# Kernel optimization log

Measured on AMD Instinct MI355X. Metric: run time of the kernel, lower is better.

The kernel has to match this reference:

```python
import jax, jax.numpy as jnp
import numpy as np

DN = ('NCHW', 'OIHW', 'NCHW')


def _conv_bn_relu(x, w, s, b):
    # ConvModule in eval mode: conv(no bias) + BN(running stats, folded to affine) + ReLU
    y = jax.lax.conv_general_dilated(x, w, (1, 1), ((1, 1), (1, 1)), dimension_numbers=DN)
    return jnp.maximum(y * s[None, :, None, None] + b[None, :, None, None], 0.0)


def _head(x, w1, s1, b1, w2, s2, b2, wf, bf):
    y = _conv_bn_relu(x, w1, s1, b1)
    y = _conv_bn_relu(y, w2, s2, b2)
    y = jax.lax.conv_general_dilated(y, wf, (1, 1), ((0, 0), (0, 0)), dimension_numbers=DN)
    return y + bf[None, :, None, None]  # [B, 5, H, W]


def _make_anchors(shapes, strides, offset=0.5):
    pts, sts = [], []
    for (h, w), s in zip(shapes, strides):
        sx = jnp.arange(w, dtype=jnp.float32) + offset
        sy = jnp.arange(h, dtype=jnp.float32) + offset
        yy, xx = jnp.meshgrid(sy, sx, indexing='ij')
        pts.append(jnp.stack((xx, yy), -1).reshape(-1, 2))
        sts.append(jnp.full((h * w, 1), float(s), dtype=jnp.float32))
    # transposed as in the torch code: anchors [2, N], strides [1, N]
    return jnp.concatenate(pts).T, jnp.concatenate(sts).T


def setup_inputs():
    key = jax.random.key(0)
    ks = jax.random.split(key, 16)
    B = 8
    cfg = {'p3': (128, 160), 'p4': (256, 80), 'p5': (512, 40)}
    inp = {}
    i = 0
    for name, (C, HW) in cfg.items():
        inp[name] = jax.random.normal(ks[i], (B, C, HW, HW), dtype=jnp.float32)
        i += 1
    for name, (C, HW) in cfg.items():
        fan3 = 1.0 / float(np.sqrt(C * 9))
        fan1 = 1.0 / float(np.sqrt(C))
        inp[f'w1_{name}'] = jax.random.normal(ks[i], (C, C, 3, 3), jnp.float32) * fan3; i += 1
        inp[f's1_{name}'] = jnp.ones((C,), jnp.float32)
        inp[f'b1_{name}'] = jnp.zeros((C,), jnp.float32)
        inp[f'w2_{name}'] = jax.random.normal(ks[i], (C, C, 3, 3), jnp.float32) * fan3; i += 1
        inp[f's2_{name}'] = jnp.ones((C,), jnp.float32)
        inp[f'b2_{name}'] = jnp.zeros((C,), jnp.float32)
        inp[f'wf_{name}'] = jax.random.normal(ks[i], (5, C, 1, 1), jnp.float32) * fan1; i += 1
        inp[f'bf_{name}'] = jnp.zeros((5,), jnp.float32)
    return inp


def reference(p3, p4, p5,
              w1_p3, s1_p3, b1_p3, w2_p3, s2_p3, b2_p3, wf_p3, bf_p3,
              w1_p4, s1_p4, b1_p4, w2_p4, s2_p4, b2_p4, wf_p4, bf_p4,
              w1_p5, s1_p5, b1_p5, w2_p5, s2_p5, b2_p5, wf_p5, bf_p5):
    y3 = _head(p3, w1_p3, s1_p3, b1_p3, w2_p3, s2_p3, b2_p3, wf_p3, bf_p3)
    y4 = _head(p4, w1_p4, s1_p4, b1_p4, w2_p4, s2_p4, b2_p4, wf_p4, bf_p4)
    y5 = _head(p5, w1_p5, s1_p5, b1_p5, w2_p5, s2_p5, b2_p5, wf_p5, bf_p5)
    feats = [y3, y4, y5]
    B = p3.shape[0]
    shapes = [(f.shape[2], f.shape[3]) for f in feats]
    anchors, strides = _make_anchors(shapes, (8, 16, 32))  # [2,N], [1,N]
    out = jnp.concatenate([f.reshape(B, 5, -1) for f in feats], axis=2)  # [B,5,N]
    box, cls = out[:, :4], out[:, 4:5]
    anc = anchors[None]  # [1,2,N]
    lt, rb = box[:, :2], box[:, 2:4]
    x1y1 = anc - lt
    x2y2 = anc + rb
    box = jnp.concatenate(((x1y1 + x2y2) * 0.5, x2y2 - x1y1), axis=1) * strides[None]
    return jnp.concatenate((box, jax.nn.sigmoid(cls)), axis=1)  # [B,5,N] pre-NMS detections
```

## Files before the change

kernel.cpp:

```cpp
#include <hip/hip_runtime.h>
#include <stdint.h>

typedef short short8 __attribute__((ext_vector_type(8)));
typedef float f32x16 __attribute__((ext_vector_type(16)));

template<int I> struct IC { static constexpr int value = I; };

__device__ __forceinline__ uint16_t f2bf(float f){
  union{float f;uint32_t u;}v; v.f=f;
  uint32_t u=v.u; u += 0x7fffu + ((u>>16)&1u);
  return (uint16_t)(u>>16);
}
__device__ __forceinline__ float bf2f(uint16_t h){
  union{uint32_t u;float f;}v; v.u=((uint32_t)h)<<16; return v.f;
}

__device__ __forceinline__ void gl_lds16(const void* g, void* l){
  __builtin_amdgcn_global_load_lds((__attribute__((address_space(1))) const void*)g,
                                   (__attribute__((address_space(3))) void*)l, 16, 0, 0);
}

__global__ __launch_bounds__(256) void prep_w(const float* __restrict__ w,
                                              const float* __restrict__ s,
                                              uint16_t* __restrict__ dst, int C){
  int idx = blockIdx.x*256 + threadIdx.x;
  int total = C*C*9;
  if (idx >= total) return;
  int tap = idx % 9; int t = idx/9;
  int ci = t % C; int co = t / C;
  float val = w[idx]*s[co];
  int KB = C>>5;
  int f = co>>5;
  int lane = (co&31) | (((ci>>3)&1)<<5);
  int kk = (ci>>4)&1, kb = ci>>5, j = ci&7;
  size_t off = ((((size_t)(f*KB + kb)*9 + tap)*2 + kk)*64 + lane)*8 + j;
  dst[off] = f2bf(val);
}

template<int C,int H>
__global__ __launch_bounds__(256) void pad_in(const float* __restrict__ x, uint16_t* __restrict__ xp){
  constexpr int W=H, Hp=H+2, Wp=W+2, KB=C/32;
  int idx = blockIdx.x*256 + threadIdx.x;
  int total = 8*KB*Hp*Wp;
  if (idx >= total) return;
  int w = idx % Wp; int t2 = idx / Wp;
  int h = t2 % Hp;  int bk = t2 / Hp;
  const uint32_t key = (uint32_t)((w&7)<<4);
  char* dst = (char*)xp;
  size_t cbyte = (size_t)idx*64;
  if (h==0 || h==Hp-1 || w==0 || w==Wp-1){
    uint4 z = {0,0,0,0};
#pragma unroll
    for (int q=0;q<4;++q) *(uint4*)(dst + ((cbyte + (uint32_t)(q*16)) ^ key)) = z;
  } else {
    const int b = bk/KB, kb = bk - b*KB;
    const float* src = x + (((size_t)(b*C + kb*32)*H + (h-1))*W + (w-1));
#pragma unroll
    for (int q=0;q<4;++q){
      uint16_t tmp[8];
#pragma unroll
      for (int j=0;j<8;++j) tmp[j] = f2bf(src[(size_t)(q*8+j)*(H*W)]);
      *(uint4*)(dst + ((cbyte + (uint32_t)(q*16)) ^ key)) = *(uint4*)tmp;
    }
  }
}

template<int C,int H>
__global__ __launch_bounds__(256) void zero_border(uint16_t* __restrict__ yp){
  constexpr int Hp=H+2, Wp=H+2, KB=C/32;
  constexpr int NB = 2*Wp + 2*(Hp-2);
  int idx = blockIdx.x*256 + threadIdx.x;
  int total = 8*KB*NB;
  if (idx >= total) return;
  int j = idx % NB; int bk = idx / NB;
  int h, w;
  if (j < 2*Wp){ h = (j<Wp)?0:(Hp-1); w = j%Wp; }
  else { int j2 = j - 2*Wp; h = 1 + (j2 % (Hp-2)); w = (j2 < (Hp-2))?0:(Wp-1); }
  size_t chunk = ((size_t)bk*Hp + h)*Wp + w;
  const uint32_t key = (uint32_t)((w&7)<<4);
  uint4 z = {0,0,0,0};
  char* dst = (char*)yp;
#pragma unroll
  for (int q=0;q<4;++q) *(uint4*)(dst + ((chunk*64 + (uint32_t)(q*16)) ^ key)) = z;
}

template<int C,int H,bool PADOUT>
__device__ __forceinline__ void conv_body(int lbid,
    const uint16_t* __restrict__ in, const uint16_t* __restrict__ wq,
    const float* __restrict__ bias, uint16_t* __restrict__ out, char* lds)
{
  constexpr int W=H, Hp=H+2, Wp=W+2, KB=C/32, TW=40, TH=8;
  constexpr int COB=128;
  constexpr int R=TH+2, BUF=R*3072, NT=R*3, WAVES=4;
  const int tid = threadIdx.x, lane = tid&63, wave = tid>>6;
  const int wm = wave>>1, wn = wave&1;
  const int l31 = lane&31, h5 = lane>>5;

  int t = lbid;
  const int cb = t % (C/COB); t /= (C/COB);
  const int wt = t % (W/TW);  t /= (W/TW);
  const int ht = t % (H/TH);
  const int b  = t / (H/TH);
  const int h0 = ht*TH, w0 = wt*TW;
  const int cbCO = cb*(COB/32);

  int addrB[5][3];
#pragma unroll
  for (int ni=0; ni<5; ++ni){
    int s = wn*160 + ni*32 + l31;
    int th = s/40, tw = s - th*40;
#pragma unroll
    for (int dw=0; dw<3; ++dw){
      int col = tw + dw;
      addrB[ni][dw] = th*3072 + ((col*64 + h5*16) ^ ((col&7)<<4));
    }
  }

  const char* wp[2];
#pragma unroll
  for (int mi=0; mi<2; ++mi){
    int f = cbCO + wm*2 + mi;
    wp[mi] = (const char*)wq + (size_t)f * ((size_t)KB*9*2*1024) + lane*16;
  }

  f32x16 acc[2][5];
#pragma unroll
  for (int mi=0;mi<2;++mi)
#pragma unroll
    for (int ni=0;ni<5;++ni)
#pragma unroll
      for (int e=0;e<16;++e) acc[mi][ni][e] = 0.f;

  auto STAGE = [&](int bi, int kb){
    const char* src = (const char*)(in + ((size_t)(b*KB + kb)*Hp + h0)*((size_t)Wp*32) + (size_t)w0*32);
    for (int tt = wave; tt < NT; tt += WAVES){
      int r = tt/3, k = tt - r*3;
      char* l = lds + bi*BUF + r*3072 + k*1024;
      const char* g = src + (size_t)r*(Wp*64) + k*1024 + lane*16;
      if (k < 2 || lane < 40) gl_lds16(g, l);
    }
  };

  auto COMPUTE = [&](auto BC){
    constexpr int BI = decltype(BC)::value;
    const char* lb = lds + BI*BUF;
    short8 wc[2][2], wnx[2][2];
#pragma unroll
    for (int mi=0;mi<2;++mi){
      wc[mi][0] = *(const short8*)(wp[mi]);
      wc[mi][1] = *(const short8*)(wp[mi] + 1024);
      wp[mi] += 2048;
    }
#pragma unroll
    for (int tap=0; tap<9; ++tap){
      const int dh = tap/3, dw = tap - dh*3;
      if (tap < 8){
#pragma unroll
        for (int mi=0;mi<2;++mi){
          wnx[mi][0] = *(const short8*)(wp[mi]);
          wnx[mi][1] = *(const short8*)(wp[mi] + 1024);
          wp[mi] += 2048;
        }
      }
#pragma unroll
      for (int ni=0; ni<5; ++ni){
        const int a0 = addrB[ni][dw] + dh*3072;
        short8 b0 = *(const short8*)(lb + a0);
        short8 b1 = *(const short8*)(lb + (a0 ^ 32));
        acc[0][ni] = __builtin_amdgcn_mfma_f32_32x32x16_bf16(wc[0][0], b0, acc[0][ni], 0,0,0);
        acc[1][ni] = __builtin_amdgcn_mfma_f32_32x32x16_bf16(wc[1][0], b0, acc[1][ni], 0,0,0);
        acc[0][ni] = __builtin_amdgcn_mfma_f32_32x32x16_bf16(wc[0][1], b1, acc[0][ni], 0,0,0);
        acc[1][ni] = __builtin_amdgcn_mfma_f32_32x32x16_bf16(wc[1][1], b1, acc[1][ni], 0,0,0);
      }
      if (tap < 8){
#pragma unroll
        for (int mi=0;mi<2;++mi){ wc[mi][0]=wnx[mi][0]; wc[mi][1]=wnx[mi][1]; }
      }
    }
  };

  STAGE(0, 0);
  __syncthreads();
#pragma unroll 1
  for (int kb = 0; kb < KB; kb += 2){
    STAGE(1, kb+1);
    COMPUTE(IC<0>{});
    __syncthreads();
    if (kb+2 < KB) STAGE(0, kb+2);
    COMPUTE(IC<1>{});
    __syncthreads();
  }

#pragma unroll
  for (int mi=0; mi<2; ++mi){
    const int kbo = cbCO + wm*2 + mi;
#pragma unroll
    for (int ni=0; ni<5; ++ni){
      const int s = wn*160 + ni*32 + l31;
      const int th = s/40, tw = s - th*40;
      size_t chunk; uint32_t key;
      if (PADOUT){
        const int hh = h0+th+1, ww = w0+tw+1;
        chunk = ((size_t)(b*KB + kbo)*Hp + hh)*Wp + ww;
        key = (uint32_t)((ww&7)<<4);
      } else {
        const int hh = h0+th, ww = w0+tw;
        chunk = ((size_t)(b*KB + kbo)*H + hh)*W + ww;
        key = (uint32_t)((ww&7)<<4);
      }
      char* ob = (char*)out;
#pragma unroll
      for (int q=0; q<4; ++q){
        const int cob = kbo*32 + q*8 + h5*4;
        float v0 = fmaxf(acc[mi][ni][4*q+0] + bias[cob+0], 0.f);
        float v1 = fmaxf(acc[mi][ni][4*q+1] + bias[cob+1], 0.f);
        float v2 = fmaxf(acc[mi][ni][4*q+2] + bias[cob+2], 0.f);
        float v3 = fmaxf(acc[mi][ni][4*q+3] + bias[cob+3], 0.f);
        uint2 dd;
        dd.x = (uint32_t)f2bf(v0) | ((uint32_t)f2bf(v1)<<16);
        dd.y = (uint32_t)f2bf(v2) | ((uint32_t)f2bf(v3)<<16);
        *(uint2*)(ob + ((chunk*64 + (uint32_t)(q*16 + h5*8)) ^ key)) = dd;
      }
    }
  }
}

template<bool PADOUT>
__global__ __launch_bounds__(256, 2) void conv_all(int b45, int b34,
    const uint16_t* in5, const uint16_t* wq5, const float* bi5, uint16_t* o5,
    const uint16_t* in4, const uint16_t* wq4, const float* bi4, uint16_t* o4,
    const uint16_t* in3, const uint16_t* wq3, const float* bi3, uint16_t* o3)
{
  __shared__ __align__(16) char lds[61440];
  const int bid = blockIdx.x;
  if (bid < b45)      conv_body<512, 40, PADOUT>(bid,       in5, wq5, bi5, o5, lds);
  else if (bid < b34) conv_body<256, 80, PADOUT>(bid - b45, in4, wq4, bi4, o4, lds);
  else                conv_body<128,160, PADOUT>(bid - b34, in3, wq3, bi3, o3, lds);
}

template<int C,int H,int OFF,int STRIDE>
__global__ __launch_bounds__(256) void head_final(const uint16_t* __restrict__ y,
    const float* __restrict__ wf, const float* __restrict__ bfp, float* __restrict__ outp)
{
  constexpr int W=H, HW=H*W, KBo=C/32, S=33600;
  int idx = blockIdx.x*256 + threadIdx.x;
  if (idx >= 8*HW) return;
  const int b = idx/HW, sp = idx - b*HW;
  const int w = sp % W;
  const uint32_t key = (uint32_t)((w&7)<<4);
  float a0=bfp[0], a1=bfp[1], a2=bfp[2], a3=bfp[3], a4=bfp[4];
  const char* yb = (const char*)y;
  for (int kb=0; kb<KBo; ++kb){
    size_t cbyte = ((size_t)(b*KBo + kb)*HW + sp)*64;
#pragma unroll
    for (int q=0; q<4; ++q){
      uint4 u = *(const uint4*)(yb + ((cbyte + (uint32_t)(q*16)) ^ key));
      const uint16_t* pv = (const uint16_t*)&u;
#pragma unroll
      for (int j=0; j<8; ++j){
        float v = bf2f(pv[j]);
        int ci = kb*32 + q*8 + j;
        a0 += v*wf[0*C+ci]; a1 += v*wf[1*C+ci]; a2 += v*wf[2*C+ci];
        a3 += v*wf[3*C+ci]; a4 += v*wf[4*C+ci];
      }
    }
  }
  const float ax = (float)(sp % W) + 0.5f;
  const float ay = (float)(sp / W) + 0.5f;
  const float o0 = (ax + 0.5f*(a2-a0)) * (float)STRIDE;
  const float o1 = (ay + 0.5f*(a3-a1)) * (float)STRIDE;
  const float o2 = (a0+a2) * (float)STRIDE;
  const float o3 = (a1+a3) * (float)STRIDE;
  const float o4 = 1.0f/(1.0f + expf(-a4));
  float* ob = outp + (size_t)b*5*S + OFF + sp;
  ob[0*S]=o0; ob[1*S]=o1; ob[2*S]=o2; ob[3*S]=o3; ob[4*S]=o4;
}

extern "C" void kernel_launch(void* const* d_in, const int* in_sizes, int n_in,
                              void* d_out, int out_size, void* d_ws, size_t ws_size,
                              hipStream_t stream){
  (void)in_sizes; (void)n_in; (void)out_size;
  const float* x[3] = {(const float*)d_in[0], (const float*)d_in[1], (const float*)d_in[2]};
  const float *w1[3],*s1[3],*b1[3],*w2[3],*s2[3],*b2[3],*wf[3],*bfp[3];
  for (int h=0; h<3; ++h){
    const int base = 3 + h*8;
    w1[h]=(const float*)d_in[base+0]; s1[h]=(const float*)d_in[base+1];
    b1[h]=(const float*)d_in[base+2]; w2[h]=(const float*)d_in[base+3];
    s2[h]=(const float*)d_in[base+4]; b2[h]=(const float*)d_in[base+5];
    wf[h]=(const float*)d_in[base+6]; bfp[h]=(const float*)d_in[base+7];
  }
  static const int   Cs[3] = {128, 256, 512};
  static const size_t Wb[3] = {294912, 1179648, 4718592};
  static const size_t Ab[3] = {53747712, 27541504, 14450688};
  static const int   NB[3] = {640, 320, 160};
  float* out = (float*)d_out;
  char* ws = (char*)d_ws;

  size_t off = 0; size_t wOff[3][2];
  for (int h=0; h<3; ++h) for (int c=0; c<2; ++c){ wOff[h][c]=off; off += Wb[h]; }
  off = (off + 255) & ~(size_t)255;
  size_t aOff[3], bOff[3];
  for (int h=0; h<3; ++h){ aOff[h]=off; off += Ab[h]; }
  for (int h=0; h<3; ++h){ bOff[h]=off; off += Ab[h]; }
  const size_t fusedNeed = off;

  const size_t seqA = (2*4718592 + 255) & ~(size_t)255;
  const size_t seqB = seqA + 53747712;
  const size_t seqNeed = seqB + 53747712;

  if (ws_size >= fusedNeed){
    for (int h=0; h<3; ++h){
      int tot = 9*Cs[h]*Cs[h];
      prep_w<<<(tot+255)/256, 256, 0, stream>>>(w1[h], s1[h], (uint16_t*)(ws+wOff[h][0]), Cs[h]);
      prep_w<<<(tot+255)/256, 256, 0, stream>>>(w2[h], s2[h], (uint16_t*)(ws+wOff[h][1]), Cs[h]);
    }
    pad_in<128,160><<<3281, 256, 0, stream>>>(x[0], (uint16_t*)(ws+aOff[0]));
    pad_in<256, 80><<<1681, 256, 0, stream>>>(x[1], (uint16_t*)(ws+aOff[1]));
    pad_in<512, 40><<< 882, 256, 0, stream>>>(x[2], (uint16_t*)(ws+aOff[2]));
    zero_border<128,160><<<81, 256, 0, stream>>>((uint16_t*)(ws+bOff[0]));
    zero_border<256, 80><<<81, 256, 0, stream>>>((uint16_t*)(ws+bOff[1]));
    zero_border<512, 40><<<82, 256, 0, stream>>>((uint16_t*)(ws+bOff[2]));
    const int b45 = NB[2], b34 = NB[2]+NB[1], grid = NB[2]+NB[1]+NB[0];
    conv_all<true><<<grid, 256, 0, stream>>>(b45, b34,
      (const uint16_t*)(ws+aOff[2]), (const uint16_t*)(ws+wOff[2][0]), b1[2], (uint16_t*)(ws+bOff[2]),
      (const uint16_t*)(ws+aOff[1]), (const uint16_t*)(ws+wOff[1][0]), b1[1], (uint16_t*)(ws+bOff[1]),
      (const uint16_t*)(ws+aOff[0]), (const uint16_t*)(ws+wOff[0][0]), b1[0], (uint16_t*)(ws+bOff[0]));
    conv_all<false><<<grid, 256, 0, stream>>>(b45, b34,
      (const uint16_t*)(ws+bOff[2]), (const uint16_t*)(ws+wOff[2][1]), b2[2], (uint16_t*)(ws+aOff[2]),
      (const uint16_t*)(ws+bOff[1]), (const uint16_t*)(ws+wOff[1][1]), b2[1], (uint16_t*)(ws+aOff[1]),
      (const uint16_t*)(ws+bOff[0]), (const uint16_t*)(ws+wOff[0][1]), b2[0], (uint16_t*)(ws+aOff[0]));
    head_final<128,160,     0,  8><<<800, 256, 0, stream>>>((const uint16_t*)(ws+aOff[0]), wf[0], bfp[0], out);
    head_final<256, 80, 25600, 16><<<200, 256, 0, stream>>>((const uint16_t*)(ws+aOff[1]), wf[1], bfp[1], out);
    head_final<512, 40, 32000, 32><<< 50, 256, 0, stream>>>((const uint16_t*)(ws+aOff[2]), wf[2], bfp[2], out);
  } else {
    if (ws_size < seqNeed) return;
    uint16_t* W1p = (uint16_t*)(ws + 0);
    uint16_t* W2p = (uint16_t*)(ws + 4718592);
    uint16_t* A   = (uint16_t*)(ws + seqA);
    uint16_t* B   = (uint16_t*)(ws + seqB);
    for (int h=0; h<3; ++h){
      int tot = 9*Cs[h]*Cs[h];
      prep_w<<<(tot+255)/256, 256, 0, stream>>>(w1[h], s1[h], W1p, Cs[h]);
      prep_w<<<(tot+255)/256, 256, 0, stream>>>(w2[h], s2[h], W2p, Cs[h]);
      int grid = NB[h];
      int b45, b34;
      if (h==2){ b45=grid; b34=grid; } else if (h==1){ b45=0; b34=grid; } else { b45=0; b34=0; }
      if (h==0){
        pad_in<128,160><<<3281,256,0,stream>>>(x[0], A);
        zero_border<128,160><<<81,256,0,stream>>>(B);
      } else if (h==1){
        pad_in<256,80><<<1681,256,0,stream>>>(x[1], A);
        zero_border<256,80><<<81,256,0,stream>>>(B);
      } else {
        pad_in<512,40><<<882,256,0,stream>>>(x[2], A);
        zero_border<512,40><<<82,256,0,stream>>>(B);
      }
      conv_all<true><<<grid, 256, 0, stream>>>(b45, b34,
        A, W1p, b1[h], B,  A, W1p, b1[h], B,  A, W1p, b1[h], B);
      conv_all<false><<<grid, 256, 0, stream>>>(b45, b34,
        B, W2p, b2[h], A,  B, W2p, b2[h], A,  B, W2p, b2[h], A);
      if (h==0)      head_final<128,160,     0,  8><<<800,256,0,stream>>>(A, wf[0], bfp[0], out);
      else if (h==1) head_final<256, 80, 25600, 16><<<200,256,0,stream>>>(A, wf[1], bfp[1], out);
      else           head_final<512, 40, 32000, 32><<< 50,256,0,stream>>>(A, wf[2], bfp[2], out);
    }
  }
}
```

Measured before the change: 848.1 us.

## Switch conv to 16x16x32 MFMA with smaller tiles and LDS-staged weight prep

Replaces the 32x32x16 bf16 MFMA tiling with 16x16x32 MFMA. Each wave now holds a 4x5 grid of 4-wide accumulators, and the spatial tile height is halved from 8 to 4 rows, which doubles the block count. The weight layout is changed to a tap-major, 16-output-channel-fragment format. A new prep kernel stages weights through LDS and writes packed bf16 pairs. Lower LDS use and fewer accumulator registers allow launch bounds of 3 blocks per CU for more occupancy, at the cost of more halo reloads per output and different MFMA throughput characteristics.

```diff
diff --git a/kernel.cpp b/kernel.cpp
--- a/kernel.cpp
+++ b/kernel.cpp
@@ -2,7 +2,7 @@
 #include <stdint.h>
 
 typedef short short8 __attribute__((ext_vector_type(8)));
-typedef float f32x16 __attribute__((ext_vector_type(16)));
+typedef float f32x4 __attribute__((ext_vector_type(4)));
 
 template<int I> struct IC { static constexpr int value = I; };
 
@@ -20,21 +20,35 @@
                                    (__attribute__((address_space(3))) void*)l, 16, 0, 0);
 }
 
-__global__ __launch_bounds__(256) void prep_w(const float* __restrict__ w,
-                                              const float* __restrict__ s,
-                                              uint16_t* __restrict__ dst, int C){
-  int idx = blockIdx.x*256 + threadIdx.x;
-  int total = C*C*9;
-  if (idx >= total) return;
-  int tap = idx % 9; int t = idx/9;
-  int ci = t % C; int co = t / C;
-  float val = w[idx]*s[co];
-  int KB = C>>5;
-  int f = co>>5;
-  int lane = (co&31) | (((ci>>3)&1)<<5);
-  int kk = (ci>>4)&1, kb = ci>>5, j = ci&7;
-  size_t off = ((((size_t)(f*KB + kb)*9 + tap)*2 + kk)*64 + lane)*8 + j;
-  dst[off] = f2bf(val);
+__global__ __launch_bounds__(256) void prep_w2(const float* __restrict__ w,
+                                               const float* __restrict__ s,
+                                               uint16_t* __restrict__ dst, int C){
+  __shared__ float lds[16][289];
+  const int F16 = C >> 4;
+  const int tid = threadIdx.x;
+  const int f16 = blockIdx.x % F16;
+  const int kb  = blockIdx.x / F16;
+#pragma unroll
+  for (int i = 0; i < 18; ++i){
+    int idx = tid + i*256;
+    int co  = idx / 288, rem = idx - co*288;
+    lds[co][rem] = w[(size_t)(f16*16 + co)*C*9 + (size_t)kb*288 + rem];
+  }
+  __syncthreads();
+  const int lane = tid >> 2;
+  const int jj   = (tid & 3)*2;
+  const int co_l = lane & 15, oct = lane >> 4;
+  const int ci0  = oct*8 + jj;
+  const float sc = s[f16*16 + co_l];
+  uint32_t* db = (uint32_t*)dst;
+#pragma unroll
+  for (int tap = 0; tap < 9; ++tap){
+    float v0 = lds[co_l][(ci0  )*9 + tap] * sc;
+    float v1 = lds[co_l][(ci0+1)*9 + tap] * sc;
+    uint32_t pk = (uint32_t)f2bf(v0) | ((uint32_t)f2bf(v1) << 16);
+    size_t o = (((size_t)(kb*9 + tap)*F16 + f16)*512 + (size_t)lane*8 + jj) >> 1;
+    db[o] = pk;
+  }
 }
 
 template<int C,int H>
@@ -89,12 +103,13 @@
     const uint16_t* __restrict__ in, const uint16_t* __restrict__ wq,
     const float* __restrict__ bias, uint16_t* __restrict__ out, char* lds)
 {
-  constexpr int W=H, Hp=H+2, Wp=W+2, KB=C/32, TW=40, TH=8;
-  constexpr int COB=128;
-  constexpr int R=TH+2, BUF=R*3072, NT=R*3, WAVES=4;
+  constexpr int W=H, Hp=H+2, Wp=W+2, KB=C/32, TW=40, TH=4;
+  constexpr int COB=128, F16B=C/16;
+  constexpr int R=TH+2, ROWB=42*64, BUF=R*ROWB, NT=R*3, WAVES=4;
+  constexpr int TAPSTRIDE = F16B*1024;
   const int tid = threadIdx.x, lane = tid&63, wave = tid>>6;
   const int wm = wave>>1, wn = wave&1;
-  const int l31 = lane&31, h5 = lane>>5;
+  const int l15 = lane&15, h2 = lane>>4;
 
   int t = lbid;
   const int cb = t % (C/COB); t /= (C/COB);
@@ -102,40 +117,38 @@
   const int ht = t % (H/TH);
   const int b  = t / (H/TH);
   const int h0 = ht*TH, w0 = wt*TW;
-  const int cbCO = cb*(COB/32);
 
   int addrB[5][3];
 #pragma unroll
   for (int ni=0; ni<5; ++ni){
-    int s = wn*160 + ni*32 + l31;
+    int s = wn*80 + ni*16 + l15;
     int th = s/40, tw = s - th*40;
 #pragma unroll
     for (int dw=0; dw<3; ++dw){
       int col = tw + dw;
-      addrB[ni][dw] = th*3072 + ((col*64 + h5*16) ^ ((col&7)<<4));
-    }
-  }
-
-  const char* wp[2];
-#pragma unroll
-  for (int mi=0; mi<2; ++mi){
-    int f = cbCO + wm*2 + mi;
-    wp[mi] = (const char*)wq + (size_t)f * ((size_t)KB*9*2*1024) + lane*16;
-  }
-
-  f32x16 acc[2][5];
-#pragma unroll
-  for (int mi=0;mi<2;++mi)
+      addrB[ni][dw] = th*ROWB + ((col*64 + h2*16) ^ ((col&7)<<4));
+    }
+  }
+
+  const char* wp = (const char*)wq + (size_t)(cb*8 + wm*4)*1024 + (size_t)lane*16;
+
+  f32x4 acc[4][5];
+#pragma unroll
+  for (int mi=0;mi<4;++mi)
 #pragma unroll
     for (int ni=0;ni<5;++ni)
-#pragma unroll
-      for (int e=0;e<16;++e) acc[mi][ni][e] = 0.f;
+      acc[mi][ni] = (f32x4){0.f,0.f,0.f,0.f};
+
+  short8 a_[4];
+#pragma unroll
+  for (int mi=0; mi<4; ++mi) a_[mi] = *(const short8*)(wp + mi*1024);
+  wp += TAPSTRIDE;
 
   auto STAGE = [&](int bi, int kb){
     const char* src = (const char*)(in + ((size_t)(b*KB + kb)*Hp + h0)*((size_t)Wp*32) + (size_t)w0*32);
     for (int tt = wave; tt < NT; tt += WAVES){
       int r = tt/3, k = tt - r*3;
-      char* l = lds + bi*BUF + r*3072 + k*1024;
+      char* l = lds + bi*BUF + r*ROWB + k*1024;
       const char* g = src + (size_t)r*(Wp*64) + k*1024 + lane*16;
       if (k < 2 || lane < 40) gl_lds16(g, l);
     }
@@ -144,38 +157,24 @@
   auto COMPUTE = [&](auto BC){
     constexpr int BI = decltype(BC)::value;
     const char* lb = lds + BI*BUF;
-    short8 wc[2][2], wnx[2][2];
-#pragma unroll
-    for (int mi=0;mi<2;++mi){
-      wc[mi][0] = *(const short8*)(wp[mi]);
-      wc[mi][1] = *(const short8*)(wp[mi] + 1024);
-      wp[mi] += 2048;
-    }
 #pragma unroll
     for (int tap=0; tap<9; ++tap){
       const int dh = tap/3, dw = tap - dh*3;
-      if (tap < 8){
-#pragma unroll
-        for (int mi=0;mi<2;++mi){
-          wnx[mi][0] = *(const short8*)(wp[mi]);
-          wnx[mi][1] = *(const short8*)(wp[mi] + 1024);
-          wp[mi] += 2048;
-        }
-      }
-#pragma unroll
-      for (int ni=0; ni<5; ++ni){
-        const int a0 = addrB[ni][dw] + dh*3072;
-        short8 b0 = *(const short8*)(lb + a0);
-        short8 b1 = *(const short8*)(lb + (a0 ^ 32));
-        acc[0][ni] = __builtin_amdgcn_mfma_f32_32x32x16_bf16(wc[0][0], b0, acc[0][ni], 0,0,0);
-        acc[1][ni] = __builtin_amdgcn_mfma_f32_32x32x16_bf16(wc[1][0], b0, acc[1][ni], 0,0,0);
-        acc[0][ni] = __builtin_amdgcn_mfma_f32_32x32x16_bf16(wc[0][1], b1, acc[0][ni], 0,0,0);
-        acc[1][ni] = __builtin_amdgcn_mfma_f32_32x32x16_bf16(wc[1][1], b1, acc[1][ni], 0,0,0);
-      }
-      if (tap < 8){
-#pragma unroll
-        for (int mi=0;mi<2;++mi){ wc[mi][0]=wnx[mi][0]; wc[mi][1]=wnx[mi][1]; }
-      }
+      short8 an_[4];
+#pragma unroll
+      for (int mi=0;mi<4;++mi) an_[mi] = *(const short8*)(wp + mi*1024);
+      wp += TAPSTRIDE;
+      short8 bf[5];
+#pragma unroll
+      for (int ni=0; ni<5; ++ni)
+        bf[ni] = *(const short8*)(lb + addrB[ni][dw] + dh*ROWB);
+#pragma unroll
+      for (int ni=0; ni<5; ++ni)
+#pragma unroll
+        for (int mi=0; mi<4; ++mi)
+          acc[mi][ni] = __builtin_amdgcn_mfma_f32_16x16x32_bf16(a_[mi], bf[ni], acc[mi][ni], 0,0,0);
+#pragma unroll
+      for (int mi=0;mi<4;++mi) a_[mi] = an_[mi];
     }
   };
 
@@ -192,11 +191,13 @@
   }
 
 #pragma unroll
-  for (int mi=0; mi<2; ++mi){
-    const int kbo = cbCO + wm*2 + mi;
+  for (int mi=0; mi<4; ++mi){
+    const int kbo = cb*4 + wm*2 + (mi>>1);
+    const int cobase = kbo*32 + (mi&1)*16 + h2*4;
+    const f32x4 bv = *(const f32x4*)(bias + cobase);
 #pragma unroll
     for (int ni=0; ni<5; ++ni){
-      const int s = wn*160 + ni*32 + l31;
+      const int s = wn*80 + ni*16 + l15;
       const int th = s/40, tw = s - th*40;
       size_t chunk; uint32_t key;
       if (PADOUT){
@@ -208,30 +209,25 @@
         chunk = ((size_t)(b*KB + kbo)*H + hh)*W + ww;
         key = (uint32_t)((ww&7)<<4);
       }
-      char* ob = (char*)out;
-#pragma unroll
-      for (int q=0; q<4; ++q){
-        const int cob = kbo*32 + q*8 + h5*4;
-        float v0 = fmaxf(acc[mi][ni][4*q+0] + bias[cob+0], 0.f);
-        float v1 = fmaxf(acc[mi][ni][4*q+1] + bias[cob+1], 0.f);
-        float v2 = fmaxf(acc[mi][ni][4*q+2] + bias[cob+2], 0.f);
-        float v3 = fmaxf(acc[mi][ni][4*q+3] + bias[cob+3], 0.f);
-        uint2 dd;
-        dd.x = (uint32_t)f2bf(v0) | ((uint32_t)f2bf(v1)<<16);
-        dd.y = (uint32_t)f2bf(v2) | ((uint32_t)f2bf(v3)<<16);
-        *(uint2*)(ob + ((chunk*64 + (uint32_t)(q*16 + h5*8)) ^ key)) = dd;
-      }
+      float v0 = fmaxf(acc[mi][ni][0] + bv[0], 0.f);
+      float v1 = fmaxf(acc[mi][ni][1] + bv[1], 0.f);
+      float v2 = fmaxf(acc[mi][ni][2] + bv[2], 0.f);
+      float v3 = fmaxf(acc[mi][ni][3] + bv[3], 0.f);
+      uint2 dd;
+      dd.x = (uint32_t)f2bf(v0) | ((uint32_t)f2bf(v1)<<16);
+      dd.y = (uint32_t)f2bf(v2) | ((uint32_t)f2bf(v3)<<16);
+      *(uint2*)((char*)out + ((chunk*64 + (uint32_t)((mi&1)*32 + h2*8)) ^ key)) = dd;
     }
   }
 }
 
 template<bool PADOUT>
-__global__ __launch_bounds__(256, 2) void conv_all(int b45, int b34,
+__global__ __launch_bounds__(256, 3) void conv_all(int b45, int b34,
     const uint16_t* in5, const uint16_t* wq5, const float* bi5, uint16_t* o5,
     const uint16_t* in4, const uint16_t* wq4, const float* bi4, uint16_t* o4,
     const uint16_t* in3, const uint16_t* wq3, const float* bi3, uint16_t* o3)
 {
-  __shared__ __align__(16) char lds[61440];
+  __shared__ __align__(16) char lds[2*6*2688];
   const int bid = blockIdx.x;
   if (bid < b45)      conv_body<512, 40, PADOUT>(bid,       in5, wq5, bi5, o5, lds);
   else if (bid < b34) conv_body<256, 80, PADOUT>(bid - b45, in4, wq4, bi4, o4, lds);
@@ -292,7 +288,7 @@
   static const int   Cs[3] = {128, 256, 512};
   static const size_t Wb[3] = {294912, 1179648, 4718592};
   static const size_t Ab[3] = {53747712, 27541504, 14450688};
-  static const int   NB[3] = {640, 320, 160};
+  static const int   NB[3] = {1280, 640, 320};
   float* out = (float*)d_out;
   char* ws = (char*)d_ws;
 
@@ -310,9 +306,9 @@
 
   if (ws_size >= fusedNeed){
     for (int h=0; h<3; ++h){
-      int tot = 9*Cs[h]*Cs[h];
-      prep_w<<<(tot+255)/256, 256, 0, stream>>>(w1[h], s1[h], (uint16_t*)(ws+wOff[h][0]), Cs[h]);
-      prep_w<<<(tot+255)/256, 256, 0, stream>>>(w2[h], s2[h], (uint16_t*)(ws+wOff[h][1]), Cs[h]);
+      int blocks = (Cs[h]/32)*(Cs[h]/16);
+      prep_w2<<<blocks, 256, 0, stream>>>(w1[h], s1[h], (uint16_t*)(ws+wOff[h][0]), Cs[h]);
+      prep_w2<<<blocks, 256, 0, stream>>>(w2[h], s2[h], (uint16_t*)(ws+wOff[h][1]), Cs[h]);
     }
     pad_in<128,160><<<3281, 256, 0, stream>>>(x[0], (uint16_t*)(ws+aOff[0]));
     pad_in<256, 80><<<1681, 256, 0, stream>>>(x[1], (uint16_t*)(ws+aOff[1]));
@@ -339,9 +335,9 @@
     uint16_t* A   = (uint16_t*)(ws + seqA);
     uint16_t* B   = (uint16_t*)(ws + seqB);
     for (int h=0; h<3; ++h){
-      int tot = 9*Cs[h]*Cs[h];
-      prep_w<<<(tot+255)/256, 256, 0, stream>>>(w1[h], s1[h], W1p, Cs[h]);
-      prep_w<<<(tot+255)/256, 256, 0, stream>>>(w2[h], s2[h], W2p, Cs[h]);
+      int blocks = (Cs[h]/32)*(Cs[h]/16);
+      prep_w2<<<blocks, 256, 0, stream>>>(w1[h], s1[h], W1p, Cs[h]);
+      prep_w2<<<blocks, 256, 0, stream>>>(w2[h], s2[h], W2p, Cs[h]);
       int grid = NB[h];
       int b45, b34;
       if (h==2){ b45=grid; b34=grid; } else if (h==1){ b45=0; b34=grid; } else { b45=0; b34=0; }
```

New measurement: 707.9 us. -16.5%, faster.
